# Kernel tuning notes

Measured on AMD Instinct MI355X. Metric: run time of the kernel, lower is better.

Reference implementation:

```python
import jax, jax.numpy as jnp
import numpy as np

B = 1
FRAMES = 16
P = 64            # patch_dim = image_size // patch_size = 256 // 4
C = 512           # query_dim == hidden_dim
T, HW, WW = 2, 8, 8   # window_size
NH = 8            # num_heads
HD = C // NH      # head_dim = 64
N = FRAMES * P * P


def setup_inputs() -> dict:
    key = jax.random.key(0)
    ks = jax.random.split(key, 5)
    x = jax.random.normal(ks[0], (B, N, C), dtype=jnp.float32)
    Wq = jax.random.normal(ks[1], (C, C), dtype=jnp.float32) * 0.02
    Wk = jax.random.normal(ks[2], (C, C), dtype=jnp.float32) * 0.02
    Wv = jax.random.normal(ks[3], (C, C), dtype=jnp.float32) * 0.02
    Wo = jax.random.normal(ks[4], (C, C), dtype=jnp.float32) * 0.02
    bo = jnp.zeros((C,), dtype=jnp.float32)
    return {"x": x, "Wq": Wq, "Wk": Wk, "Wv": Wv, "Wo": Wo, "bo": bo}


def reference(x, Wq, Wk, Wv, Wo, bo):
    nT, nH, nW = FRAMES // T, P // HW, P // WW
    L = T * HW * WW            # tokens per window = 128
    NWIN = nT * nH * nW        # 512 windows

    # window partition: [B,N,C] -> [B,nWin,L,C]
    xw = x.reshape(B, nT, T, nH, HW, nW, WW, C)
    xw = xw.transpose(0, 1, 3, 5, 2, 4, 6, 7).reshape(B, NWIN, L, C)

    # QKV projections (torch Linear: y = x @ W.T), split heads
    q = (xw @ Wq.T).reshape(B, NWIN, L, NH, HD)
    k = (xw @ Wk.T).reshape(B, NWIN, L, NH, HD)
    v = (xw @ Wv.T).reshape(B, NWIN, L, NH, HD)

    scale = 1.0 / jnp.sqrt(jnp.float32(HD))
    attn = jnp.einsum('bwqhd,bwkhd->bwhqk', q, k) * scale
    attn = jax.nn.softmax(attn, axis=-1)
    out = jnp.einsum('bwhqk,bwkhd->bwqhd', attn, v).reshape(B, NWIN, L, C)

    out = out @ Wo.T + bo      # output projection (dropout is identity at p=0/eval)

    # window merge: inverse of partition
    y = out.reshape(B, nT, nH, nW, T, HW, WW, C)
    y = y.transpose(0, 1, 4, 2, 5, 3, 6, 7).reshape(B, N, C)
    return y
```

## Files before the change

kernel.cpp:

```cpp
#include <hip/hip_runtime.h>


typedef __bf16 bf16x8 __attribute__((ext_vector_type(8)));
typedef float  f32x4  __attribute__((ext_vector_type(4)));

__device__ __forceinline__ unsigned short f2bf(float f) {
    unsigned int u = __float_as_uint(f);
    u += 0x7FFFu + ((u >> 16) & 1u);
    return (unsigned short)(u >> 16);
}
__device__ __forceinline__ unsigned int pack2(float lo, float hi) {
    return (unsigned int)f2bf(lo) | ((unsigned int)f2bf(hi) << 16);
}
__device__ __forceinline__ void glds16(const void* g, void* l) {
    __builtin_amdgcn_global_load_lds(
        (const __attribute__((address_space(1))) unsigned int*)g,
        (__attribute__((address_space(3))) unsigned int*)l, 16, 0, 0);
}

__global__ __launch_bounds__(256) void gather_cvt(const float* __restrict__ x,
                                                  unsigned short* __restrict__ xbf) {
    int tid = blockIdx.x * 256 + threadIdx.x;
    int r = tid >> 6;
    int c = (tid & 63) << 3;
    int w = r >> 7, l = r & 127;
    int wt = w >> 6, wy = (w >> 3) & 7, wx = w & 7;
    int lt = l >> 6, ly = (l >> 3) & 7, lx = l & 7;
    size_t n = (size_t)(wt * 2 + lt) * 4096 + (size_t)(wy * 8 + ly) * 64 + (wx * 8 + lx);
    const float4* s = (const float4*)(x + n * 512 + c);
    float4 a = s[0], b = s[1];
    uint4 o;
    o.x = pack2(a.x, a.y); o.y = pack2(a.z, a.w);
    o.z = pack2(b.x, b.y); o.w = pack2(b.z, b.w);
    *(uint4*)(xbf + (size_t)r * 512 + c) = o;
}

__global__ __launch_bounds__(256) void cvt_w4(const float* __restrict__ Wq,
                                              const float* __restrict__ Wk,
                                              const float* __restrict__ Wv,
                                              const float* __restrict__ Wo,
                                              unsigned short* __restrict__ d) {
    int b = blockIdx.x >> 7;
    int tid = (blockIdx.x & 127) * 256 + threadIdx.x;
    const float* s = (b == 0) ? Wq : (b == 1) ? Wk : (b == 2) ? Wv : Wo;
    const float4* sp = (const float4*)s + (size_t)tid * 2;
    float4 a = sp[0], bb = sp[1];
    uint4 o;
    o.x = pack2(a.x, a.y); o.y = pack2(a.z, a.w);
    o.z = pack2(bb.x, bb.y); o.w = pack2(bb.z, bb.w);
    ((uint4*)(d + (size_t)b * 262144))[tid] = o;
}

__global__ __launch_bounds__(256, 2) void qkv_gemm(const unsigned short* __restrict__ xbf,
                                                   const unsigned short* __restrict__ wb,
                                                   unsigned short* __restrict__ Qb,
                                                   unsigned short* __restrict__ Kb,
                                                   unsigned short* __restrict__ Vb) {
    int id = blockIdx.x;
    int xcd = id & 7, rest = id >> 3;
    int w = xcd * 64 + (rest >> 2);
    int nb = rest & 3;
    const unsigned short* A = xbf + (size_t)w * 128 * 512;
    const unsigned short* B0 = wb + (size_t)nb * 128 * 512;
    __shared__ unsigned short sA[128 * 64];
    __shared__ unsigned short sB[3][128 * 64];
    f32x4 acc[3][4][4] = {};
    int t = threadIdx.x, lane = t & 63, wv = t >> 6;
    int wm = wv & 1, wn = wv >> 1, quad = lane >> 4, lc = lane & 15;
    int sw = lc & 7;

    int sr = t >> 3;
    int gco = ((t & 7) ^ (sr & 7)) * 8;

    for (int k0 = 0; k0 < 512; k0 += 64) {
        __syncthreads();
        #pragma unroll
        for (int i = 0; i < 4; i++) {
            int r = sr + i * 32;
            glds16(A + (size_t)r * 512 + k0 + gco, sA + (t + i * 256) * 8);
            #pragma unroll
            for (int pj = 0; pj < 3; pj++)
                glds16(B0 + pj * 262144 + (size_t)r * 512 + k0 + gco,
                       sB[pj] + (t + i * 256) * 8);
        }
        __syncthreads();
        #pragma unroll
        for (int ks = 0; ks < 2; ks++) {
            int ch = ((quad + ks * 4) ^ sw) * 8;
            bf16x8 af[4];
            #pragma unroll
            for (int i = 0; i < 4; i++)
                af[i] = *(const bf16x8*)(&sA[(wm * 64 + i * 16 + lc) * 64 + ch]);
            #pragma unroll
            for (int pj = 0; pj < 3; pj++)
                #pragma unroll
                for (int ni = 0; ni < 4; ni++) {
                    bf16x8 bfr = *(const bf16x8*)(&sB[pj][(wn * 64 + ni * 16 + lc) * 64 + ch]);
                    #pragma unroll
                    for (int mi = 0; mi < 4; mi++)
                        acc[pj][mi][ni] = __builtin_amdgcn_mfma_f32_16x16x32_bf16(af[mi], bfr, acc[pj][mi][ni], 0, 0, 0);
                }
        }
    }

    int c0 = nb * 128 + wn * 64;
    #pragma unroll
    for (int mi = 0; mi < 4; mi++)
        #pragma unroll
        for (int ni = 0; ni < 4; ni++)
            #pragma unroll
            for (int rg = 0; rg < 4; rg++) {
                int col = c0 + ni * 16 + lc;
                int h = col >> 6, d = col & 63;
                int l = wm * 64 + mi * 16 + quad * 4 + rg;
                Qb[(((size_t)w * 8 + h) * 128 + l) * 64 + d] = f2bf(acc[0][mi][ni][rg] * 0.125f);
                Kb[(((size_t)w * 8 + h) * 128 + l) * 64 + d] = f2bf(acc[1][mi][ni][rg]);
                Vb[(((size_t)w * 8 + h) * 64 + d) * 128 + l] = f2bf(acc[2][mi][ni][rg]);
            }
}

__global__ __launch_bounds__(256) void attn(const unsigned short* __restrict__ Qb,
                                            const unsigned short* __restrict__ Kb,
                                            const unsigned short* __restrict__ Vb,
                                            unsigned short* __restrict__ O) {
    int h = blockIdx.x, w = blockIdx.y;
    size_t base = ((size_t)w * 8 + h) * 8192;
    const unsigned short* q = Qb + base;
    const unsigned short* k = Kb + base;
    const unsigned short* v = Vb + base;

    __shared__ unsigned short smem[24576];
    unsigned short* sV = smem;
    unsigned short* sQ = smem + 8192;
    unsigned short* sK = smem + 16384;
    unsigned short* sP = smem + 8192;

    int t = threadIdx.x, lane = t & 63, wv = t >> 6;
    int quad = lane >> 4, lc = lane & 15;
    int sw = lc & 7;

    #pragma unroll
    for (int i = 0; i < 4; i++) {
        int s = t + i * 256;
        int r = s >> 3;
        int cq = ((s & 7) ^ (r & 7)) * 8;
        glds16(q + (size_t)r * 64 + cq, sQ + s * 8);
        glds16(k + (size_t)r * 64 + cq, sK + s * 8);
        int rv = s >> 4;
        int cv = (((s & 15) ^ (rv & 7))) * 8;
        glds16(v + (size_t)rv * 128 + cv, sV + s * 8);
    }
    __syncthreads();

    f32x4 acc[2][8] = {};
    #pragma unroll
    for (int ks = 0; ks < 2; ks++) {
        int ch = ((quad + ks * 4) ^ sw) * 8;
        bf16x8 af[2];
        #pragma unroll
        for (int mi = 0; mi < 2; mi++)
            af[mi] = *(const bf16x8*)(&sQ[(wv * 32 + mi * 16 + lc) * 64 + ch]);
        #pragma unroll
        for (int ni = 0; ni < 8; ni++) {
            bf16x8 bfr = *(const bf16x8*)(&sK[(ni * 16 + lc) * 64 + ch]);
            #pragma unroll
            for (int mi = 0; mi < 2; mi++)
                acc[mi][ni] = __builtin_amdgcn_mfma_f32_16x16x32_bf16(af[mi], bfr, acc[mi][ni], 0, 0, 0);
        }
    }

    #pragma unroll
    for (int mi = 0; mi < 2; mi++)
        #pragma unroll
        for (int rg = 0; rg < 4; rg++) {
            float m = -1e30f;
            #pragma unroll
            for (int ni = 0; ni < 8; ni++) m = fmaxf(m, acc[mi][ni][rg]);
            #pragma unroll
            for (int off = 1; off < 16; off <<= 1) m = fmaxf(m, __shfl_xor(m, off, 64));
            float s = 0.f;
            #pragma unroll
            for (int ni = 0; ni < 8; ni++) {
                float e = __expf(acc[mi][ni][rg] - m);
                acc[mi][ni][rg] = e;
                s += e;
            }
            #pragma unroll
            for (int off = 1; off < 16; off <<= 1) s += __shfl_xor(s, off, 64);
            float inv = 1.0f / s;
            #pragma unroll
            for (int ni = 0; ni < 8; ni++) acc[mi][ni][rg] *= inv;
        }

    __syncthreads();
    #pragma unroll
    for (int mi = 0; mi < 2; mi++)
        #pragma unroll
        for (int ni = 0; ni < 8; ni++)
            #pragma unroll
            for (int rg = 0; rg < 4; rg++) {
                int r = wv * 32 + mi * 16 + quad * 4 + rg;
                int c = ni * 16 + lc;
                sP[r * 128 + (((c >> 3) ^ (r & 7)) << 3) + (c & 7)] = f2bf(acc[mi][ni][rg]);
            }
    __syncthreads();

    f32x4 oc[2][4] = {};
    #pragma unroll
    for (int ks = 0; ks < 4; ks++) {
        int ch = ((quad + ks * 4) ^ sw) * 8;
        bf16x8 af[2];
        #pragma unroll
        for (int mi = 0; mi < 2; mi++)
            af[mi] = *(const bf16x8*)(&sP[(wv * 32 + mi * 16 + lc) * 128 + ch]);
        #pragma unroll
        for (int ni = 0; ni < 4; ni++) {
            bf16x8 bfr = *(const bf16x8*)(&sV[(ni * 16 + lc) * 128 + ch]);
            #pragma unroll
            for (int mi = 0; mi < 2; mi++)
                oc[mi][ni] = __builtin_amdgcn_mfma_f32_16x16x32_bf16(af[mi], bfr, oc[mi][ni], 0, 0, 0);
        }
    }

    #pragma unroll
    for (int mi = 0; mi < 2; mi++)
        #pragma unroll
        for (int ni = 0; ni < 4; ni++)
            #pragma unroll
            for (int rg = 0; rg < 4; rg++) {
                int l = wv * 32 + mi * 16 + quad * 4 + rg;
                int d = ni * 16 + lc;
                O[((size_t)w * 128 + l) * 512 + h * 64 + d] = f2bf(oc[mi][ni][rg]);
            }
}

__global__ __launch_bounds__(256) void oproj_gemm(const unsigned short* __restrict__ A,
                                                  const unsigned short* __restrict__ Bw,
                                                  const float* __restrict__ bo,
                                                  float* __restrict__ out) {
    int id = blockIdx.x;
    int xcd = id & 7, rest = id >> 3;
    int rb = xcd * 64 + (rest >> 2);
    int nb = rest & 3;
    const unsigned short* Ab = A + (size_t)rb * 128 * 512;
    const unsigned short* Bb = Bw + (size_t)nb * 128 * 512;
    __shared__ unsigned short sA[128 * 64];
    __shared__ unsigned short sB[128 * 64];
    f32x4 acc[4][4] = {};
    int t = threadIdx.x, lane = t & 63, wv = t >> 6;
    int wm = wv & 1, wn = wv >> 1, quad = lane >> 4, lc = lane & 15;
    int sw = lc & 7;

    int sr = t >> 3;
    int gco = ((t & 7) ^ (sr & 7)) * 8;

    for (int k0 = 0; k0 < 512; k0 += 64) {
        __syncthreads();
        #pragma unroll
        for (int i = 0; i < 4; i++) {
            int r = sr + i * 32;
            glds16(Ab + (size_t)r * 512 + k0 + gco, sA + (t + i * 256) * 8);
            glds16(Bb + (size_t)r * 512 + k0 + gco, sB + (t + i * 256) * 8);
        }
        __syncthreads();
        #pragma unroll
        for (int ks = 0; ks < 2; ks++) {
            int ch = ((quad + ks * 4) ^ sw) * 8;
            bf16x8 af[4], bfr[4];
            #pragma unroll
            for (int i = 0; i < 4; i++) {
                af[i]  = *(const bf16x8*)(&sA[(wm * 64 + i * 16 + lc) * 64 + ch]);
                bfr[i] = *(const bf16x8*)(&sB[(wn * 64 + i * 16 + lc) * 64 + ch]);
            }
            #pragma unroll
            for (int mi = 0; mi < 4; mi++)
                #pragma unroll
                for (int ni = 0; ni < 4; ni++)
                    acc[mi][ni] = __builtin_amdgcn_mfma_f32_16x16x32_bf16(af[mi], bfr[ni], acc[mi][ni], 0, 0, 0);
        }
    }

    float bias[4];
    #pragma unroll
    for (int ni = 0; ni < 4; ni++)
        bias[ni] = bo[nb * 128 + wn * 64 + ni * 16 + lc];

    #pragma unroll
    for (int mi = 0; mi < 4; mi++)
        #pragma unroll
        for (int rg = 0; rg < 4; rg++) {
            int r = rb * 128 + wm * 64 + mi * 16 + quad * 4 + rg;
            int w = r >> 7, l = r & 127;
            int wt = w >> 6, wy = (w >> 3) & 7, wx = w & 7;
            int lt = l >> 6, ly = (l >> 3) & 7, lx = l & 7;
            size_t n = (size_t)(wt * 2 + lt) * 4096 + (size_t)(wy * 8 + ly) * 64 + (wx * 8 + lx);
            #pragma unroll
            for (int ni = 0; ni < 4; ni++) {
                int col = nb * 128 + wn * 64 + ni * 16 + lc;
                out[n * 512 + col] = acc[mi][ni][rg] + bias[ni];
            }
        }
}

extern "C" void kernel_launch(void* const* d_in, const int* in_sizes, int n_in,
                              void* d_out, int out_size, void* d_ws, size_t ws_size,
                              hipStream_t stream) {
    const float* x  = (const float*)d_in[0];
    const float* Wq = (const float*)d_in[1];
    const float* Wk = (const float*)d_in[2];
    const float* Wv = (const float*)d_in[3];
    const float* Wo = (const float*)d_in[4];
    const float* bo = (const float*)d_in[5];
    float* out = (float*)d_out;

    char* ws = (char*)d_ws;
    unsigned short* xbf = (unsigned short*)(ws);
    unsigned short* Qb  = (unsigned short*)(ws + 67108864);
    unsigned short* Kb  = (unsigned short*)(ws + 134217728);
    unsigned short* Vb  = (unsigned short*)(ws + 201326592);
    unsigned short* Wqb = (unsigned short*)(ws + 268435456);

    gather_cvt<<<16384, 256, 0, stream>>>(x, xbf);
    cvt_w4<<<512, 256, 0, stream>>>(Wq, Wk, Wv, Wo, Wqb);

    qkv_gemm<<<2048, 256, 0, stream>>>(xbf, Wqb, Qb, Kb, Vb);
    attn<<<dim3(8, 512), 256, 0, stream>>>(Qb, Kb, Vb, xbf);
    oproj_gemm<<<2048, 256, 0, stream>>>(xbf, Wqb + 786432, bo, out);
}
```

Before: 478.0 us.

## Rewrite QKV GEMM as 256x256-tile, 8-wave, double-buffered pipelined kernel

Replaces the 128-row by 3x128-column QKV GEMM with a 512-thread kernel that computes 256x256 output tiles. K-slices are double-buffered in 128KB of dynamic LDS, and global-to-LDS loads are interleaved with MFMA phases using explicit waitcnt, barriers and setprio. The goal is to hide load latency and raise arithmetic intensity per block. It needs a large LDS allocation, which limits occupancy, and depends on carefully hand-tuned wait counts being correct.

```diff
diff --git a/kernel.cpp b/kernel.cpp
--- a/kernel.cpp
+++ b/kernel.cpp
@@ -51,72 +51,126 @@
     ((uint4*)(d + (size_t)b * 262144))[tid] = o;
 }
 
-__global__ __launch_bounds__(256, 2) void qkv_gemm(const unsigned short* __restrict__ xbf,
-                                                   const unsigned short* __restrict__ wb,
-                                                   unsigned short* __restrict__ Qb,
-                                                   unsigned short* __restrict__ Kb,
-                                                   unsigned short* __restrict__ Vb) {
+
+#define STAGE_A(tt, kh) do {                                                   \
+    const unsigned short* g_ = Ap + (size_t)(tt) * 64 + (kh) * 32 + gOff;      \
+    unsigned short* l_ = smem + ((((tt) & 1) * 2 + (kh)) * 8192);              \
+    glds16(g_, l_ + j * 8);                                                    \
+    glds16(g_ + 65536, l_ + 4096 + j * 8);                                     \
+  } while (0)
+
+#define STAGE_B(tt, kh) do {                                                   \
+    const unsigned short* g_ = Bp + (size_t)(tt) * 64 + (kh) * 32 + gOff;      \
+    unsigned short* l_ = smem + 32768 + ((((tt) & 1) * 2 + (kh)) * 8192);      \
+    glds16(g_, l_ + j * 8);                                                    \
+    glds16(g_ + 65536, l_ + 4096 + j * 8);                                     \
+  } while (0)
+
+#define PH_READA(d, ks, mh)                                                    \
+    _Pragma("unroll") for (int i_ = 0; i_ < 4; ++i_)                           \
+      af[i_] = *(const bf16x8*)(smem + ((d) * 2 + (ks)) * 8192 +               \
+                                (arow + (mh) * 64 + i_ * 16) * 32 + ech);
+
+#define PH_READB(d, ks)                                                        \
+    _Pragma("unroll") for (int n_ = 0; n_ < 4; ++n_)                           \
+      bfr[n_] = *(const bf16x8*)(smem + 32768 + ((d) * 2 + (ks)) * 8192 +      \
+                                 (brow + n_ * 16) * 32 + ech);
+
+#define PH_MFMA(mh)                                                            \
+    __builtin_amdgcn_s_barrier();                                              \
+    asm volatile("s_waitcnt lgkmcnt(0)" ::: "memory");                         \
+    __builtin_amdgcn_sched_barrier(0);                                         \
+    __builtin_amdgcn_s_setprio(1);                                             \
+    _Pragma("unroll") for (int n_ = 0; n_ < 4; ++n_)                           \
+      _Pragma("unroll") for (int i_ = 0; i_ < 4; ++i_)                         \
+        acc[(mh) * 4 + i_][n_] = __builtin_amdgcn_mfma_f32_16x16x32_bf16(      \
+            af[i_], bfr[n_], acc[(mh) * 4 + i_][n_], 0, 0, 0);                 \
+    __builtin_amdgcn_s_setprio(0);                                             \
+    __builtin_amdgcn_s_barrier();
+
+__global__ __launch_bounds__(512, 2) void qkv_gemm8(const unsigned short* __restrict__ xbf,
+                                                    const unsigned short* __restrict__ wb,
+                                                    unsigned short* __restrict__ Qb,
+                                                    unsigned short* __restrict__ Kb,
+                                                    unsigned short* __restrict__ Vb) {
+    extern __shared__ unsigned short smem[];
     int id = blockIdx.x;
     int xcd = id & 7, rest = id >> 3;
-    int w = xcd * 64 + (rest >> 2);
-    int nb = rest & 3;
-    const unsigned short* A = xbf + (size_t)w * 128 * 512;
-    const unsigned short* B0 = wb + (size_t)nb * 128 * 512;
-    __shared__ unsigned short sA[128 * 64];
-    __shared__ unsigned short sB[3][128 * 64];
-    f32x4 acc[3][4][4] = {};
-    int t = threadIdx.x, lane = t & 63, wv = t >> 6;
-    int wm = wv & 1, wn = wv >> 1, quad = lane >> 4, lc = lane & 15;
-    int sw = lc & 7;
-
-    int sr = t >> 3;
-    int gco = ((t & 7) ^ (sr & 7)) * 8;
-
-    for (int k0 = 0; k0 < 512; k0 += 64) {
-        __syncthreads();
-        #pragma unroll
-        for (int i = 0; i < 4; i++) {
-            int r = sr + i * 32;
-            glds16(A + (size_t)r * 512 + k0 + gco, sA + (t + i * 256) * 8);
-            #pragma unroll
-            for (int pj = 0; pj < 3; pj++)
-                glds16(B0 + pj * 262144 + (size_t)r * 512 + k0 + gco,
-                       sB[pj] + (t + i * 256) * 8);
-        }
-        __syncthreads();
-        #pragma unroll
-        for (int ks = 0; ks < 2; ks++) {
-            int ch = ((quad + ks * 4) ^ sw) * 8;
-            bf16x8 af[4];
-            #pragma unroll
-            for (int i = 0; i < 4; i++)
-                af[i] = *(const bf16x8*)(&sA[(wm * 64 + i * 16 + lc) * 64 + ch]);
-            #pragma unroll
-            for (int pj = 0; pj < 3; pj++)
+    int rowblk = xcd * 32 + rest / 6;
+    int colblk = rest % 6;
+
+    const unsigned short* Ap = xbf + (size_t)rowblk * 131072;
+    const unsigned short* Bp = wb + (size_t)colblk * 131072;
+
+    int j = threadIdx.x;
+    int lane = j & 63, wv = j >> 6;
+    int wm = wv >> 2, wn = wv & 3;
+    int quad = lane >> 4, lc = lane & 15;
+
+    int r0 = j >> 2;
+    int dcol = (((j & 3) ^ ((j >> 3) & 3)) << 3);
+    const size_t gOff = (size_t)r0 * 512 + dcol;
+
+    int arow = wm * 128 + lc;
+    int brow = wn * 64 + lc;
+    int ech = (quad ^ ((lc >> 1) & 3)) << 3;
+
+    f32x4 acc[8][4] = {};
+    bf16x8 af[4], bfr[4];
+
+    STAGE_A(0, 0); STAGE_B(0, 0); STAGE_A(0, 1); STAGE_B(0, 1);
+    STAGE_A(1, 0); STAGE_B(1, 0);
+    asm volatile("s_waitcnt vmcnt(4)" ::: "memory");
+    __builtin_amdgcn_s_barrier();
+
+    #pragma unroll 2
+    for (int t = 0; t < 8; ++t) {
+        const int d = t & 1;
+        PH_READA(d, 0, 0); PH_READB(d, 0);
+        if (t < 7) STAGE_A(t + 1, 1);
+        PH_MFMA(0);
+        PH_READA(d, 0, 1);
+        if (t < 7) STAGE_B(t + 1, 1);
+        PH_MFMA(1);
+        PH_READA(d, 1, 0); PH_READB(d, 1);
+        if (t < 6) STAGE_A(t + 2, 0);
+        PH_MFMA(0);
+        PH_READA(d, 1, 1);
+        if (t < 6) {
+            STAGE_B(t + 2, 0);
+            asm volatile("s_waitcnt vmcnt(4)" ::: "memory");
+        } else if (t == 6) {
+            asm volatile("s_waitcnt vmcnt(0)" ::: "memory");
+        }
+        PH_MFMA(1);
+    }
+
+    int cb = colblk * 256 + wn * 64;
+    int pj = cb >> 9;
+    int h = (cb >> 6) & 7;
+    int w2 = rowblk * 2 + wm;
+    size_t ob = ((size_t)w2 * 8 + h) * 8192;
+    if (pj == 2) {
+        #pragma unroll
+        for (int mi = 0; mi < 8; ++mi)
+            #pragma unroll
+            for (int n = 0; n < 4; ++n)
                 #pragma unroll
-                for (int ni = 0; ni < 4; ni++) {
-                    bf16x8 bfr = *(const bf16x8*)(&sB[pj][(wn * 64 + ni * 16 + lc) * 64 + ch]);
-                    #pragma unroll
-                    for (int mi = 0; mi < 4; mi++)
-                        acc[pj][mi][ni] = __builtin_amdgcn_mfma_f32_16x16x32_bf16(af[mi], bfr, acc[pj][mi][ni], 0, 0, 0);
-                }
-        }
-    }
-
-    int c0 = nb * 128 + wn * 64;
-    #pragma unroll
-    for (int mi = 0; mi < 4; mi++)
-        #pragma unroll
-        for (int ni = 0; ni < 4; ni++)
-            #pragma unroll
-            for (int rg = 0; rg < 4; rg++) {
-                int col = c0 + ni * 16 + lc;
-                int h = col >> 6, d = col & 63;
-                int l = wm * 64 + mi * 16 + quad * 4 + rg;
-                Qb[(((size_t)w * 8 + h) * 128 + l) * 64 + d] = f2bf(acc[0][mi][ni][rg] * 0.125f);
-                Kb[(((size_t)w * 8 + h) * 128 + l) * 64 + d] = f2bf(acc[1][mi][ni][rg]);
-                Vb[(((size_t)w * 8 + h) * 64 + d) * 128 + l] = f2bf(acc[2][mi][ni][rg]);
-            }
+                for (int rg = 0; rg < 4; ++rg)
+                    Vb[ob + (size_t)(n * 16 + lc) * 128 + (mi * 16 + quad * 4 + rg)] =
+                        f2bf(acc[mi][n][rg]);
+    } else {
+        unsigned short* outp = pj ? Kb : Qb;
+        float s = pj ? 1.0f : 0.125f;
+        #pragma unroll
+        for (int mi = 0; mi < 8; ++mi)
+            #pragma unroll
+            for (int n = 0; n < 4; ++n)
+                #pragma unroll
+                for (int rg = 0; rg < 4; ++rg)
+                    outp[ob + (size_t)(mi * 16 + quad * 4 + rg) * 64 + n * 16 + lc] =
+                        f2bf(acc[mi][n][rg] * s);
+    }
 }
 
 __global__ __launch_bounds__(256) void attn(const unsigned short* __restrict__ Qb,
@@ -320,10 +374,17 @@
     unsigned short* Vb  = (unsigned short*)(ws + 201326592);
     unsigned short* Wqb = (unsigned short*)(ws + 268435456);
 
+    static bool attrset = false;
+    if (!attrset) {
+        (void)hipFuncSetAttribute(reinterpret_cast<const void*>(qkv_gemm8),
+                                  hipFuncAttributeMaxDynamicSharedMemorySize, 131072);
+        attrset = true;
+    }
+
     gather_cvt<<<16384, 256, 0, stream>>>(x, xbf);
     cvt_w4<<<512, 256, 0, stream>>>(Wq, Wk, Wv, Wo, Wqb);
 
-    qkv_gemm<<<2048, 256, 0, stream>>>(xbf, Wqb, Qb, Kb, Vb);
+    qkv_gemm8<<<1536, 512, 131072, stream>>>(xbf, Wqb, Qb, Kb, Vb);
     attn<<<dim3(8, 512), 256, 0, stream>>>(Qb, Kb, Vb, xbf);
     oproj_gemm<<<2048, 256, 0, stream>>>(xbf, Wqb + 786432, bo, out);
 }
```

New measurement: 481.5 us. Within noise of the previous version (+0.7%).
